# Kernel optimization log

Hardware: AMD Instinct MI355X
Metric: run time of the kernel (lower is better)

The kernel has to match this reference:

```python
import jax, jax.numpy as jnp
import numpy as np

B, T = 256, 64
ACT, EMB = 6, 1024
S, D = 32, 32          # stoch, discrete
SF = S * D             # flattened stochastic state (1024)
DET, HID = 600, 600


def _st_sample(logit, g):
    """Gumbel-max categorical sample with straight-through gradient.
    logit, g: [B, S, D]. Returns one-hot sample [B, S, D]."""
    idx = jnp.argmax(logit + g, axis=-1)
    onehot = jax.nn.one_hot(idx, logit.shape[-1], dtype=logit.dtype)
    probs = jax.nn.softmax(logit, axis=-1)
    return onehot + probs - jax.lax.stop_gradient(probs)


def setup_inputs() -> dict:
    key = jax.random.key(0)
    ks = jax.random.split(key, 20)
    p = lambda k, shp: (jax.random.normal(k, shp, dtype=jnp.float32) * 0.02)
    inp = {
        "action": jax.random.normal(ks[0], (B, T, ACT), dtype=jnp.float32),
        "embed": jax.random.normal(ks[1], (B, T, EMB), dtype=jnp.float32),
        "noise_img": jax.random.gumbel(ks[2], (B, T, S, D), dtype=jnp.float32),
        "noise_obs": jax.random.gumbel(ks[3], (B, T, S, D), dtype=jnp.float32),
        # img1: Dense(hidden, elu) on concat([stoch, action])
        "W_img1": p(ks[4], (SF + ACT, HID)), "b_img1": jnp.zeros((HID,), jnp.float32),
        # keras GRUCell (reset_after=True): gate order z, r, h; two biases
        "Wx": p(ks[5], (HID, 3 * DET)), "Wh": p(ks[6], (DET, 3 * DET)),
        "b_in": jnp.zeros((3 * DET,), jnp.float32), "b_rec": jnp.zeros((3 * DET,), jnp.float32),
        # img2: Dense(hidden, elu); img5: Dense(stoch*discrete)
        "W_img2": p(ks[7], (DET, HID)), "b_img2": jnp.zeros((HID,), jnp.float32),
        "W_img5": p(ks[8], (HID, SF)), "b_img5": jnp.zeros((SF,), jnp.float32),
        # obs1: Dense(hidden, elu) on concat([deter, embed]); obs3: Dense(stoch*discrete)
        "W_obs1": p(ks[9], (DET + EMB, HID)), "b_obs1": jnp.zeros((HID,), jnp.float32),
        "W_obs3": p(ks[10], (HID, SF)), "b_obs3": jnp.zeros((SF,), jnp.float32),
    }
    return inp


def reference(action, embed, noise_img, noise_obs,
              W_img1, b_img1, Wx, Wh, b_in, b_rec,
              W_img2, b_img2, W_img5, b_img5,
              W_obs1, b_obs1, W_obs3, b_obs3):
    # initial state: zeros (RSSM.initial)
    stoch0 = jnp.zeros((B, SF), jnp.float32)
    deter0 = jnp.zeros((B, DET), jnp.float32)

    def step(carry, inp):
        stoch, deter = carry                       # [B,SF], [B,DET]
        a, e, g_img, g_obs = inp
        # ---- img_step (prior) ----
        x = jax.nn.elu(jnp.concatenate([stoch, a], -1) @ W_img1 + b_img1)  # [B,HID]
        gx = x @ Wx + b_in                         # [B,3*DET]
        gh = deter @ Wh + b_rec
        xz, xr, xh = jnp.split(gx, 3, -1)
        hz, hr, hh = jnp.split(gh, 3, -1)
        z = jax.nn.sigmoid(xz + hz)
        r = jax.nn.sigmoid(xr + hr)
        cand = jnp.tanh(xh + r * hh)
        deter_n = z * deter + (1.0 - z) * cand     # [B,DET]
        y = jax.nn.elu(deter_n @ W_img2 + b_img2)
        logit_prior = (y @ W_img5 + b_img5).reshape(B, S, D)
        stoch_prior = _st_sample(logit_prior, g_img).reshape(B, SF)
        # ---- obs_step (post) ----
        o = jax.nn.elu(jnp.concatenate([deter_n, e], -1) @ W_obs1 + b_obs1)
        logit_post = (o @ W_obs3 + b_obs3).reshape(B, S, D)
        stoch_post = _st_sample(logit_post, g_obs).reshape(B, SF)
        out = (logit_post.reshape(B, SF), stoch_post, deter_n,
               logit_prior.reshape(B, SF), stoch_prior)
        return (stoch_post, deter_n), out

    xs = (jnp.swapaxes(action, 0, 1), jnp.swapaxes(embed, 0, 1),
          jnp.swapaxes(noise_img, 0, 1), jnp.swapaxes(noise_obs, 0, 1))
    _, outs = jax.lax.scan(step, (stoch0, deter0), xs)
    # outs: each [T,B,*] -> [B,T,*]; concat post_logit|post_stoch|deter|prior_logit|prior_stoch
    out = jnp.concatenate([jnp.swapaxes(o, 0, 1) for o in outs], axis=-1)  # [B,T,4*SF+DET]
    return out
```

## Files before the change

### kernel.cpp

```cpp
#include <hip/hip_runtime.h>
#include <math.h>

namespace {

constexpr int B = 256, T = 64, ACTN = 6, EMB = 1024;
constexpr int S = 32, DD = 32, SFN = 1024;
constexpr int DET = 600, HID = 600;
constexpr int OUTF = 4 * SFN + DET;

__device__ __forceinline__ float elu1(float x) { return x > 0.f ? x : expm1f(x); }
__device__ __forceinline__ float sigm(float x) { return 1.f / (1.f + expf(-x)); }

__device__ __forceinline__ bool jgMap(int bid, int& jg, int& rg) {
    int xcd = bid & 7, slot = bid >> 3;
    int jgLocal = slot >> 2;
    rg = slot & 3;
    int cnt = (xcd < 3) ? 10 : 9;
    if (jgLocal >= cnt) return false;
    jg = ((xcd < 3) ? xcd * 10 : 30 + (xcd - 3) * 9) + jgLocal;
    return true;
}

__global__ void kWB(const float* __restrict__ Wx, const float* __restrict__ Wh,
                    float* __restrict__ WBm) {
    int k = blockIdx.x;
    const float* src = (k < 600) ? (Wx + (size_t)k * 1800) : (Wh + (size_t)(k - 600) * 1800);
    for (int j = threadIdx.x; j < 600; j += blockDim.x) {
        size_t o = ((size_t)j * 1200 + k) * 3;
        WBm[o + 0] = src[j];
        WBm[o + 1] = src[600 + j];
        WBm[o + 2] = src[1200 + j];
    }
}

__global__ void kWC(const float* __restrict__ W2, const float* __restrict__ Wo1,
                    float* __restrict__ WCm) {
    int k = blockIdx.x;
    for (int j = threadIdx.x; j < 1200; j += blockDim.x) {
        float v = (j < 600) ? W2[(size_t)k * 600 + j] : Wo1[(size_t)k * 600 + (j - 600)];
        WCm[(size_t)j * 600 + k] = v;
    }
}

__global__ void kWD(const float* __restrict__ W5, const float* __restrict__ Wo3,
                    float* __restrict__ WDm) {
    int k = blockIdx.x;
    for (int j = threadIdx.x; j < 2048; j += blockDim.x) {
        float v = (j < 1024) ? W5[(size_t)k * 1024 + j] : Wo3[(size_t)k * 1024 + (j - 1024)];
        WDm[(size_t)j * 600 + k] = v;
    }
}

__global__ __launch_bounds__(512) void kPemb(const float* __restrict__ embed,
                                             const float* __restrict__ Wo1,
                                             const float* __restrict__ bo1,
                                             float* __restrict__ embPre) {
    int bid = blockIdx.x;
    int jg = bid % 10;
    int r = bid / 10;
    int bg = r & 3;
    int t = r >> 2;
    int tid = threadIdx.x;
    int lane = tid & 63;
    int wid = __builtin_amdgcn_readfirstlane(tid >> 6);
    int b0 = bg * 64;
    int j0 = jg * 64 + wid * 8;
    bool active = (j0 < 600);
    __shared__ float tile[64 * 129];
    float acc[8] = {0, 0, 0, 0, 0, 0, 0, 0};
    for (int kc = 0; kc < EMB; kc += 128) {
        __syncthreads();
        for (int ii = tid; ii < 64 * 128; ii += 512) {
            int i = ii >> 7, k = ii & 127;
            tile[i * 129 + k] = embed[((size_t)(b0 + i) * T + t) * EMB + kc + k];
        }
        __syncthreads();
        if (active) {
            const float* wbase = Wo1 + (size_t)(600 + kc) * 600 + j0;
#pragma unroll 4
            for (int k = 0; k < 128; ++k) {
                float v = tile[lane * 129 + k];
                float4 wa = *(const float4*)(wbase + (size_t)k * 600);
                float4 wb = *(const float4*)(wbase + (size_t)k * 600 + 4);
                acc[0] += v * wa.x; acc[1] += v * wa.y; acc[2] += v * wa.z; acc[3] += v * wa.w;
                acc[4] += v * wb.x; acc[5] += v * wb.y; acc[6] += v * wb.z; acc[7] += v * wb.w;
            }
        }
    }
    if (active) {
#pragma unroll
        for (int c = 0; c < 8; ++c)
            embPre[((size_t)t * 600 + j0 + c) * B + b0 + lane] = acc[c] + bo1[j0 + c];
    }
}

__global__ __launch_bounds__(256) void kA(const float* __restrict__ act,
                                          const float* __restrict__ W1,
                                          const float* __restrict__ b1,
                                          const int* __restrict__ idxB,
                                          float* __restrict__ xT, int t, int first) {
    int b = blockIdx.x, tid = threadIdx.x;
    __shared__ float sa[ACTN];
    __shared__ int si[S];
    if (tid < ACTN) sa[tid] = act[((size_t)b * T + t) * ACTN + tid];
    if (!first && tid < S) si[tid] = idxB[b * S + tid];
    __syncthreads();
    for (int h = tid; h < HID; h += 256) {
        float a = b1[h];
#pragma unroll
        for (int k = 0; k < ACTN; ++k) a += sa[k] * W1[(size_t)(SFN + k) * HID + h];
        if (!first) {
#pragma unroll 8
            for (int s = 0; s < S; ++s) a += W1[(size_t)(s * DD + si[s]) * HID + h];
        }
        xT[(size_t)h * B + b] = elu1(a);
    }
}

__global__ __launch_bounds__(512) void kB(const float* __restrict__ xT,
                                          const float* __restrict__ dPrev,
                                          const float* __restrict__ WBm,
                                          const float* __restrict__ b_in,
                                          const float* __restrict__ b_rec,
                                          float* __restrict__ dNext,
                                          float* __restrict__ out, int t) {
    int tid = threadIdx.x, lane = tid & 63;
    int wid = __builtin_amdgcn_readfirstlane(tid >> 6);
    int jg, rg;
    if (!jgMap(blockIdx.x, jg, rg)) return;
    int j = jg * 8 + wid;
    int b = rg * 64 + lane;
    const float* w = WBm + (size_t)j * 3600;
    float az = 0, ar = 0, ax = 0, ah = 0;
#pragma unroll 2
    for (int k = 0; k < 600; k += 4) {
        float4 wa = *(const float4*)(w + 3 * k);
        float4 wb = *(const float4*)(w + 3 * k + 4);
        float4 wc = *(const float4*)(w + 3 * k + 8);
        float x0 = xT[(size_t)(k + 0) * B + b];
        float x1 = xT[(size_t)(k + 1) * B + b];
        float x2 = xT[(size_t)(k + 2) * B + b];
        float x3 = xT[(size_t)(k + 3) * B + b];
        az += x0 * wa.x + x1 * wa.w + x2 * wb.z + x3 * wc.y;
        ar += x0 * wa.y + x1 * wb.x + x2 * wb.w + x3 * wc.z;
        ax += x0 * wa.z + x1 * wb.y + x2 * wc.x + x3 * wc.w;
    }
    const float* w2 = w + 1800;
#pragma unroll 2
    for (int k = 0; k < 600; k += 4) {
        float4 wa = *(const float4*)(w2 + 3 * k);
        float4 wb = *(const float4*)(w2 + 3 * k + 4);
        float4 wc = *(const float4*)(w2 + 3 * k + 8);
        float x0 = dPrev[(size_t)(k + 0) * B + b];
        float x1 = dPrev[(size_t)(k + 1) * B + b];
        float x2 = dPrev[(size_t)(k + 2) * B + b];
        float x3 = dPrev[(size_t)(k + 3) * B + b];
        az += x0 * wa.x + x1 * wa.w + x2 * wb.z + x3 * wc.y;
        ar += x0 * wa.y + x1 * wb.x + x2 * wb.w + x3 * wc.z;
        ah += x0 * wa.z + x1 * wb.y + x2 * wc.x + x3 * wc.w;
    }
    float dp = dPrev[(size_t)j * B + b];
    float z = sigm(az + b_in[j] + b_rec[j]);
    float rr = sigm(ar + b_in[600 + j] + b_rec[600 + j]);
    float cand = tanhf(ax + b_in[1200 + j] + rr * (ah + b_rec[1200 + j]));
    float dn = z * dp + (1.f - z) * cand;
    dNext[(size_t)j * B + b] = dn;
    out[((size_t)b * T + t) * OUTF + 2 * SFN + j] = dn;
}

__global__ __launch_bounds__(512) void kC(const float* __restrict__ dT,
                                          const float* __restrict__ WCm,
                                          const float* __restrict__ b2,
                                          const float* __restrict__ embPre,
                                          float* __restrict__ yoT, int t) {
    int tid = threadIdx.x, lane = tid & 63;
    int wid = __builtin_amdgcn_readfirstlane(tid >> 6);
    int jg, rg;
    if (!jgMap(blockIdx.x, jg, rg)) return;
    int j0 = jg * 16 + wid * 2;
    int b = rg * 64 + lane;
    const float* w0 = WCm + (size_t)j0 * 600;
    const float* w1 = w0 + 600;
    float a0 = 0, a1 = 0;
#pragma unroll 2
    for (int k = 0; k < 600; k += 4) {
        float4 p = *(const float4*)(w0 + k);
        float4 q = *(const float4*)(w1 + k);
        float v0 = dT[(size_t)(k + 0) * B + b];
        float v1 = dT[(size_t)(k + 1) * B + b];
        float v2 = dT[(size_t)(k + 2) * B + b];
        float v3 = dT[(size_t)(k + 3) * B + b];
        a0 += v0 * p.x + v1 * p.y + v2 * p.z + v3 * p.w;
        a1 += v0 * q.x + v1 * q.y + v2 * q.z + v3 * q.w;
    }
    if (j0 < 600) {
        yoT[(size_t)j0 * B + b] = elu1(a0 + b2[j0]);
        yoT[(size_t)(j0 + 1) * B + b] = elu1(a1 + b2[j0 + 1]);
    } else {
        int je = j0 - 600;
        yoT[(size_t)j0 * B + b] = elu1(a0 + embPre[((size_t)t * 600 + je) * B + b]);
        yoT[(size_t)(j0 + 1) * B + b] = elu1(a1 + embPre[((size_t)t * 600 + je + 1) * B + b]);
    }
}

__global__ __launch_bounds__(512) void kD(const float* __restrict__ yoT,
                                          const float* __restrict__ WDm,
                                          const float* __restrict__ b5,
                                          const float* __restrict__ bo3,
                                          const float* __restrict__ gImg,
                                          const float* __restrict__ gObs,
                                          float* __restrict__ out,
                                          int* __restrict__ idxB, int t) {
    int tid = threadIdx.x, lane = tid & 63;
    int wid = __builtin_amdgcn_readfirstlane(tid >> 6);
    int xcd = blockIdx.x & 7, slot = blockIdx.x >> 3;
    int sg = xcd * 8 + (slot & 7);
    int rg = slot >> 3;
    int post = (sg >= 32) ? 1 : 0;
    int s = post ? sg - 32 : sg;
    int b = rg * 64 + lane;
    int dloc = wid * 4;
    int jglob = post * SFN + s * DD + dloc;
    const float* src = yoT + (post ? (size_t)600 * B : 0);
    const float* w0 = WDm + (size_t)jglob * 600;
    const float* w1 = w0 + 600;
    const float* w2 = w0 + 1200;
    const float* w3 = w0 + 1800;
    float a0 = 0, a1 = 0, a2 = 0, a3 = 0;
#pragma unroll 2
    for (int k = 0; k < 600; k += 4) {
        float4 p0 = *(const float4*)(w0 + k);
        float4 p1 = *(const float4*)(w1 + k);
        float4 p2 = *(const float4*)(w2 + k);
        float4 p3 = *(const float4*)(w3 + k);
        float v0 = src[(size_t)(k + 0) * B + b];
        float v1 = src[(size_t)(k + 1) * B + b];
        float v2 = src[(size_t)(k + 2) * B + b];
        float v3 = src[(size_t)(k + 3) * B + b];
        a0 += v0 * p0.x + v1 * p0.y + v2 * p0.z + v3 * p0.w;
        a1 += v0 * p1.x + v1 * p1.y + v2 * p1.z + v3 * p1.w;
        a2 += v0 * p2.x + v1 * p2.y + v2 * p2.z + v3 * p2.w;
        a3 += v0 * p3.x + v1 * p3.y + v2 * p3.z + v3 * p3.w;
    }
    const float* bias = post ? (bo3 + s * DD) : (b5 + s * DD);
    const float* g = (post ? gObs : gImg) + ((size_t)b * T + t) * SFN + s * DD;
    size_t obase = ((size_t)b * T + t) * OUTF;
    size_t lbase = obase + (post ? 0 : (2 * SFN + DET)) + s * DD;
    float vals[4];
    float accs[4] = {a0, a1, a2, a3};
#pragma unroll
    for (int c = 0; c < 4; ++c) {
        float lg = accs[c] + bias[dloc + c];
        out[lbase + dloc + c] = lg;
        vals[c] = lg + g[dloc + c];
    }
    float bm = vals[0];
    int bi = dloc;
#pragma unroll
    for (int c = 1; c < 4; ++c)
        if (vals[c] > bm) { bm = vals[c]; bi = dloc + c; }
    __shared__ float sm[8 * 64];
    __shared__ int sx[8 * 64];
    sm[wid * 64 + lane] = bm;
    sx[wid * 64 + lane] = bi;
    __syncthreads();
    float best = sm[lane];
    int bd = sx[lane];
#pragma unroll
    for (int w = 1; w < 8; ++w) {
        float v = sm[w * 64 + lane];
        if (v > best) { best = v; bd = sx[w * 64 + lane]; }
    }
    size_t sbase = obase + (post ? SFN : (3 * SFN + DET)) + s * DD;
#pragma unroll
    for (int c = 0; c < 4; ++c)
        out[sbase + dloc + c] = (dloc + c == bd) ? 1.f : 0.f;
    if (post && wid == 0) idxB[b * S + s] = bd;
}

}

extern "C" void kernel_launch(void* const* d_in, const int* in_sizes, int n_in,
                              void* d_out, int out_size, void* d_ws, size_t ws_size,
                              hipStream_t stream) {
    const float* action = (const float*)d_in[0];
    const float* embed  = (const float*)d_in[1];
    const float* gImg   = (const float*)d_in[2];
    const float* gObs   = (const float*)d_in[3];
    const float* W1     = (const float*)d_in[4];
    const float* b1     = (const float*)d_in[5];
    const float* Wx     = (const float*)d_in[6];
    const float* Wh     = (const float*)d_in[7];
    const float* b_in   = (const float*)d_in[8];
    const float* b_rec  = (const float*)d_in[9];
    const float* W2     = (const float*)d_in[10];
    const float* b2     = (const float*)d_in[11];
    const float* W5     = (const float*)d_in[12];
    const float* b5     = (const float*)d_in[13];
    const float* Wo1    = (const float*)d_in[14];
    const float* bo1    = (const float*)d_in[15];
    const float* Wo3    = (const float*)d_in[16];
    const float* bo3    = (const float*)d_in[17];
    float* out = (float*)d_out;

    float* ws = (float*)d_ws;
    float* WBm    = ws;
    float* WCm    = WBm + 2160000;
    float* WDm    = WCm + 720000;
    float* embPre = WDm + 1228800;
    float* xT     = embPre + 9830400;
    float* dA     = xT + 153600;
    float* dB     = dA + 153600;
    float* yoT    = dB + 153600;
    int*   idxB   = (int*)(yoT + 307200);

    hipMemsetAsync(dA, 0, 153600 * sizeof(float), stream);
    kWB<<<1200, 256, 0, stream>>>(Wx, Wh, WBm);
    kWC<<<600, 256, 0, stream>>>(W2, Wo1, WCm);
    kWD<<<600, 256, 0, stream>>>(W5, Wo3, WDm);
    kPemb<<<2560, 512, 0, stream>>>(embed, Wo1, bo1, embPre);

    for (int t = 0; t < T; ++t) {
        float* dP = (t & 1) ? dB : dA;
        float* dN = (t & 1) ? dA : dB;
        kA<<<256, 256, 0, stream>>>(action, W1, b1, idxB, xT, t, t == 0 ? 1 : 0);
        kB<<<320, 512, 0, stream>>>(xT, dP, WBm, b_in, b_rec, dN, out, t);
        kC<<<320, 512, 0, stream>>>(dN, WCm, b2, embPre, yoT, t);
        kD<<<256, 512, 0, stream>>>(yoT, WDm, b5, bo3, gImg, gObs, out, idxB, t);
    }
}
```

Before: 10.32 ms.

## Split K across two wave halves and stage activations through LDS in GEMV kernels

The three per-step matvec kernels kB, kC and kD now launch 1024-thread blocks. Each K-range is split between two groups of 8 waves, and the partial sums are reduced through shared memory. Activation columns for the block's 64 batch rows are staged into LDS in chunks of 100 rows instead of being loaded per lane from global memory. The intent is more parallelism per output and fewer redundant global activation loads, at the cost of extra barriers, an LDS reduction, and tighter register limits from launch_bounds(1024,8).

```diff
diff --git a/kernel.cpp b/kernel.cpp
--- a/kernel.cpp
+++ b/kernel.cpp
@@ -7,6 +7,7 @@
 constexpr int S = 32, DD = 32, SFN = 1024;
 constexpr int DET = 600, HID = 600;
 constexpr int OUTF = 4 * SFN + DET;
+constexpr int KC = 100;
 
 __device__ __forceinline__ float elu1(float x) { return x > 0.f ? x : expm1f(x); }
 __device__ __forceinline__ float sigm(float x) { return 1.f / (1.f + expf(-x)); }
@@ -19,6 +20,21 @@
     if (jgLocal >= cnt) return false;
     jg = ((xcd < 3) ? xcd * 10 : 30 + (xcd - 3) * 9) + jgLocal;
     return true;
+}
+
+__device__ __forceinline__ void stage2(const float* __restrict__ sA,
+                                       const float* __restrict__ sB,
+                                       float* __restrict__ tA,
+                                       float* __restrict__ tB,
+                                       int b0, int tid) {
+    for (int idx = tid; idx < KC * 16 * 2; idx += 1024) {
+        int hf = idx >= KC * 16;
+        int i2 = hf ? (idx - KC * 16) : idx;
+        int kk = i2 >> 4, q = (i2 & 15) << 2;
+        float4 v = *(const float4*)((hf ? sB : sA) + (size_t)kk * B + b0 + q);
+        float* d = (hf ? tB : tA) + kk * 64 + q;
+        d[0] = v.x; d[1] = v.y; d[2] = v.z; d[3] = v.w;
+    }
 }
 
 __global__ void kWB(const float* __restrict__ Wx, const float* __restrict__ Wh,
@@ -117,165 +133,220 @@
     }
 }
 
-__global__ __launch_bounds__(512) void kB(const float* __restrict__ xT,
-                                          const float* __restrict__ dPrev,
-                                          const float* __restrict__ WBm,
-                                          const float* __restrict__ b_in,
-                                          const float* __restrict__ b_rec,
-                                          float* __restrict__ dNext,
-                                          float* __restrict__ out, int t) {
+__global__ __launch_bounds__(1024, 8) void kB(const float* __restrict__ xT,
+                                              const float* __restrict__ dPrev,
+                                              const float* __restrict__ WBm,
+                                              const float* __restrict__ b_in,
+                                              const float* __restrict__ b_rec,
+                                              float* __restrict__ dNext,
+                                              float* __restrict__ out, int t) {
+    int jg, rg;
+    if (!jgMap(blockIdx.x, jg, rg)) return;
     int tid = threadIdx.x, lane = tid & 63;
     int wid = __builtin_amdgcn_readfirstlane(tid >> 6);
+    int ws = wid & 7, kh = wid >> 3;
+    int j = jg * 8 + ws;
+    int b0 = rg * 64;
+    int b = b0 + lane;
+    __shared__ float tA[KC * 64];
+    __shared__ float tB[KC * 64];
+    __shared__ float part[8][3][64];
+    const float* wbase = WBm + (size_t)j * 3600 + (kh ? 1800 : 0);
+    float a0 = 0, a1 = 0, a2 = 0;
+    for (int c = 0; c < 600; c += KC) {
+        stage2(xT + (size_t)c * B, dPrev + (size_t)c * B, tA, tB, b0, tid);
+        __syncthreads();
+        const float* w = wbase + 3 * c;
+        const float* tl = kh ? tB : tA;
+#pragma unroll 2
+        for (int kk = 0; kk < KC; kk += 4) {
+            float4 wa = *(const float4*)(w + 3 * kk);
+            float4 wb = *(const float4*)(w + 3 * kk + 4);
+            float4 wc = *(const float4*)(w + 3 * kk + 8);
+            float x0 = tl[(kk + 0) * 64 + lane];
+            float x1 = tl[(kk + 1) * 64 + lane];
+            float x2 = tl[(kk + 2) * 64 + lane];
+            float x3 = tl[(kk + 3) * 64 + lane];
+            a0 += x0 * wa.x + x1 * wa.w + x2 * wb.z + x3 * wc.y;
+            a1 += x0 * wa.y + x1 * wb.x + x2 * wb.w + x3 * wc.z;
+            a2 += x0 * wa.z + x1 * wb.y + x2 * wc.x + x3 * wc.w;
+        }
+        __syncthreads();
+    }
+    if (kh) {
+        part[ws][0][lane] = a0;
+        part[ws][1][lane] = a1;
+        part[ws][2][lane] = a2;
+    }
+    __syncthreads();
+    if (!kh) {
+        float az = a0 + part[ws][0][lane];
+        float ar = a1 + part[ws][1][lane];
+        float ax = a2;
+        float ah = part[ws][2][lane];
+        float dp = dPrev[(size_t)j * B + b];
+        float z = sigm(az + b_in[j] + b_rec[j]);
+        float rr = sigm(ar + b_in[600 + j] + b_rec[600 + j]);
+        float cand = tanhf(ax + b_in[1200 + j] + rr * (ah + b_rec[1200 + j]));
+        float dn = z * dp + (1.f - z) * cand;
+        dNext[(size_t)j * B + b] = dn;
+        out[((size_t)b * T + t) * OUTF + 2 * SFN + j] = dn;
+    }
+}
+
+__global__ __launch_bounds__(1024, 8) void kC(const float* __restrict__ dT,
+                                              const float* __restrict__ WCm,
+                                              const float* __restrict__ b2,
+                                              const float* __restrict__ embPre,
+                                              float* __restrict__ yoT, int t) {
     int jg, rg;
     if (!jgMap(blockIdx.x, jg, rg)) return;
-    int j = jg * 8 + wid;
-    int b = rg * 64 + lane;
-    const float* w = WBm + (size_t)j * 3600;
-    float az = 0, ar = 0, ax = 0, ah = 0;
-#pragma unroll 2
-    for (int k = 0; k < 600; k += 4) {
-        float4 wa = *(const float4*)(w + 3 * k);
-        float4 wb = *(const float4*)(w + 3 * k + 4);
-        float4 wc = *(const float4*)(w + 3 * k + 8);
-        float x0 = xT[(size_t)(k + 0) * B + b];
-        float x1 = xT[(size_t)(k + 1) * B + b];
-        float x2 = xT[(size_t)(k + 2) * B + b];
-        float x3 = xT[(size_t)(k + 3) * B + b];
-        az += x0 * wa.x + x1 * wa.w + x2 * wb.z + x3 * wc.y;
-        ar += x0 * wa.y + x1 * wb.x + x2 * wb.w + x3 * wc.z;
-        ax += x0 * wa.z + x1 * wb.y + x2 * wc.x + x3 * wc.w;
-    }
-    const float* w2 = w + 1800;
-#pragma unroll 2
-    for (int k = 0; k < 600; k += 4) {
-        float4 wa = *(const float4*)(w2 + 3 * k);
-        float4 wb = *(const float4*)(w2 + 3 * k + 4);
-        float4 wc = *(const float4*)(w2 + 3 * k + 8);
-        float x0 = dPrev[(size_t)(k + 0) * B + b];
-        float x1 = dPrev[(size_t)(k + 1) * B + b];
-        float x2 = dPrev[(size_t)(k + 2) * B + b];
-        float x3 = dPrev[(size_t)(k + 3) * B + b];
-        az += x0 * wa.x + x1 * wa.w + x2 * wb.z + x3 * wc.y;
-        ar += x0 * wa.y + x1 * wb.x + x2 * wb.w + x3 * wc.z;
-        ah += x0 * wa.z + x1 * wb.y + x2 * wc.x + x3 * wc.w;
-    }
-    float dp = dPrev[(size_t)j * B + b];
-    float z = sigm(az + b_in[j] + b_rec[j]);
-    float rr = sigm(ar + b_in[600 + j] + b_rec[600 + j]);
-    float cand = tanhf(ax + b_in[1200 + j] + rr * (ah + b_rec[1200 + j]));
-    float dn = z * dp + (1.f - z) * cand;
-    dNext[(size_t)j * B + b] = dn;
-    out[((size_t)b * T + t) * OUTF + 2 * SFN + j] = dn;
-}
-
-__global__ __launch_bounds__(512) void kC(const float* __restrict__ dT,
-                                          const float* __restrict__ WCm,
-                                          const float* __restrict__ b2,
-                                          const float* __restrict__ embPre,
-                                          float* __restrict__ yoT, int t) {
     int tid = threadIdx.x, lane = tid & 63;
     int wid = __builtin_amdgcn_readfirstlane(tid >> 6);
-    int jg, rg;
-    if (!jgMap(blockIdx.x, jg, rg)) return;
-    int j0 = jg * 16 + wid * 2;
-    int b = rg * 64 + lane;
-    const float* w0 = WCm + (size_t)j0 * 600;
+    int ws = wid & 7, kh = wid >> 3;
+    int j0 = jg * 16 + ws * 2;
+    int b0 = rg * 64;
+    int b = b0 + lane;
+    __shared__ float tA[KC * 64];
+    __shared__ float tB[KC * 64];
+    __shared__ float part[8][2][64];
+    const float* w0 = WCm + (size_t)j0 * 600 + kh * 300;
     const float* w1 = w0 + 600;
     float a0 = 0, a1 = 0;
+    for (int c = 0; c < 300; c += KC) {
+        stage2(dT + (size_t)c * B, dT + (size_t)(300 + c) * B, tA, tB, b0, tid);
+        __syncthreads();
+        const float* tl = kh ? tB : tA;
 #pragma unroll 2
-    for (int k = 0; k < 600; k += 4) {
-        float4 p = *(const float4*)(w0 + k);
-        float4 q = *(const float4*)(w1 + k);
-        float v0 = dT[(size_t)(k + 0) * B + b];
-        float v1 = dT[(size_t)(k + 1) * B + b];
-        float v2 = dT[(size_t)(k + 2) * B + b];
-        float v3 = dT[(size_t)(k + 3) * B + b];
-        a0 += v0 * p.x + v1 * p.y + v2 * p.z + v3 * p.w;
-        a1 += v0 * q.x + v1 * q.y + v2 * q.z + v3 * q.w;
-    }
-    if (j0 < 600) {
-        yoT[(size_t)j0 * B + b] = elu1(a0 + b2[j0]);
-        yoT[(size_t)(j0 + 1) * B + b] = elu1(a1 + b2[j0 + 1]);
-    } else {
-        int je = j0 - 600;
-        yoT[(size_t)j0 * B + b] = elu1(a0 + embPre[((size_t)t * 600 + je) * B + b]);
-        yoT[(size_t)(j0 + 1) * B + b] = elu1(a1 + embPre[((size_t)t * 600 + je + 1) * B + b]);
-    }
-}
-
-__global__ __launch_bounds__(512) void kD(const float* __restrict__ yoT,
-                                          const float* __restrict__ WDm,
-                                          const float* __restrict__ b5,
-                                          const float* __restrict__ bo3,
-                                          const float* __restrict__ gImg,
-                                          const float* __restrict__ gObs,
-                                          float* __restrict__ out,
-                                          int* __restrict__ idxB, int t) {
+        for (int kk = 0; kk < KC; kk += 4) {
+            float4 p = *(const float4*)(w0 + c + kk);
+            float4 q = *(const float4*)(w1 + c + kk);
+            float v0 = tl[(kk + 0) * 64 + lane];
+            float v1 = tl[(kk + 1) * 64 + lane];
+            float v2 = tl[(kk + 2) * 64 + lane];
+            float v3 = tl[(kk + 3) * 64 + lane];
+            a0 += v0 * p.x + v1 * p.y + v2 * p.z + v3 * p.w;
+            a1 += v0 * q.x + v1 * q.y + v2 * q.z + v3 * q.w;
+        }
+        __syncthreads();
+    }
+    if (kh) {
+        part[ws][0][lane] = a0;
+        part[ws][1][lane] = a1;
+    }
+    __syncthreads();
+    if (!kh) {
+        float s0 = a0 + part[ws][0][lane];
+        float s1 = a1 + part[ws][1][lane];
+        if (j0 < 600) {
+            yoT[(size_t)j0 * B + b] = elu1(s0 + b2[j0]);
+            yoT[(size_t)(j0 + 1) * B + b] = elu1(s1 + b2[j0 + 1]);
+        } else {
+            int je = j0 - 600;
+            yoT[(size_t)j0 * B + b] = elu1(s0 + embPre[((size_t)t * 600 + je) * B + b]);
+            yoT[(size_t)(j0 + 1) * B + b] = elu1(s1 + embPre[((size_t)t * 600 + je + 1) * B + b]);
+        }
+    }
+}
+
+__global__ __launch_bounds__(1024, 4) void kD(const float* __restrict__ yoT,
+                                              const float* __restrict__ WDm,
+                                              const float* __restrict__ b5,
+                                              const float* __restrict__ bo3,
+                                              const float* __restrict__ gImg,
+                                              const float* __restrict__ gObs,
+                                              float* __restrict__ out,
+                                              int* __restrict__ idxB, int t) {
     int tid = threadIdx.x, lane = tid & 63;
     int wid = __builtin_amdgcn_readfirstlane(tid >> 6);
+    int ws = wid & 7, kh = wid >> 3;
     int xcd = blockIdx.x & 7, slot = blockIdx.x >> 3;
     int sg = xcd * 8 + (slot & 7);
     int rg = slot >> 3;
     int post = (sg >= 32) ? 1 : 0;
     int s = post ? sg - 32 : sg;
-    int b = rg * 64 + lane;
-    int dloc = wid * 4;
+    int b0 = rg * 64;
+    int b = b0 + lane;
+    int dloc = ws * 4;
     int jglob = post * SFN + s * DD + dloc;
     const float* src = yoT + (post ? (size_t)600 * B : 0);
-    const float* w0 = WDm + (size_t)jglob * 600;
+    __shared__ float tA[KC * 64];
+    __shared__ float tB[KC * 64];
+    __shared__ float part[8][4][64];
+    __shared__ float sm[8 * 64];
+    __shared__ int sx[8 * 64];
+    const float* w0 = WDm + (size_t)jglob * 600 + kh * 300;
     const float* w1 = w0 + 600;
     const float* w2 = w0 + 1200;
     const float* w3 = w0 + 1800;
     float a0 = 0, a1 = 0, a2 = 0, a3 = 0;
+    for (int c = 0; c < 300; c += KC) {
+        stage2(src + (size_t)c * B, src + (size_t)(300 + c) * B, tA, tB, b0, tid);
+        __syncthreads();
+        const float* tl = kh ? tB : tA;
 #pragma unroll 2
-    for (int k = 0; k < 600; k += 4) {
-        float4 p0 = *(const float4*)(w0 + k);
-        float4 p1 = *(const float4*)(w1 + k);
-        float4 p2 = *(const float4*)(w2 + k);
-        float4 p3 = *(const float4*)(w3 + k);
-        float v0 = src[(size_t)(k + 0) * B + b];
-        float v1 = src[(size_t)(k + 1) * B + b];
-        float v2 = src[(size_t)(k + 2) * B + b];
-        float v3 = src[(size_t)(k + 3) * B + b];
-        a0 += v0 * p0.x + v1 * p0.y + v2 * p0.z + v3 * p0.w;
-        a1 += v0 * p1.x + v1 * p1.y + v2 * p1.z + v3 * p1.w;
-        a2 += v0 * p2.x + v1 * p2.y + v2 * p2.z + v3 * p2.w;
-        a3 += v0 * p3.x + v1 * p3.y + v2 * p3.z + v3 * p3.w;
-    }
-    const float* bias = post ? (bo3 + s * DD) : (b5 + s * DD);
-    const float* g = (post ? gObs : gImg) + ((size_t)b * T + t) * SFN + s * DD;
-    size_t obase = ((size_t)b * T + t) * OUTF;
-    size_t lbase = obase + (post ? 0 : (2 * SFN + DET)) + s * DD;
-    float vals[4];
-    float accs[4] = {a0, a1, a2, a3};
-#pragma unroll
-    for (int c = 0; c < 4; ++c) {
-        float lg = accs[c] + bias[dloc + c];
-        out[lbase + dloc + c] = lg;
-        vals[c] = lg + g[dloc + c];
-    }
-    float bm = vals[0];
-    int bi = dloc;
-#pragma unroll
-    for (int c = 1; c < 4; ++c)
-        if (vals[c] > bm) { bm = vals[c]; bi = dloc + c; }
-    __shared__ float sm[8 * 64];
-    __shared__ int sx[8 * 64];
-    sm[wid * 64 + lane] = bm;
-    sx[wid * 64 + lane] = bi;
+        for (int kk = 0; kk < KC; kk += 4) {
+            float4 p0 = *(const float4*)(w0 + c + kk);
+            float4 p1 = *(const float4*)(w1 + c + kk);
+            float4 p2 = *(const float4*)(w2 + c + kk);
+            float4 p3 = *(const float4*)(w3 + c + kk);
+            float v0 = tl[(kk + 0) * 64 + lane];
+            float v1 = tl[(kk + 1) * 64 + lane];
+            float v2 = tl[(kk + 2) * 64 + lane];
+            float v3 = tl[(kk + 3) * 64 + lane];
+            a0 += v0 * p0.x + v1 * p0.y + v2 * p0.z + v3 * p0.w;
+            a1 += v0 * p1.x + v1 * p1.y + v2 * p1.z + v3 * p1.w;
+            a2 += v0 * p2.x + v1 * p2.y + v2 * p2.z + v3 * p2.w;
+            a3 += v0 * p3.x + v1 * p3.y + v2 * p3.z + v3 * p3.w;
+        }
+        __syncthreads();
+    }
+    if (kh) {
+        part[ws][0][lane] = a0;
+        part[ws][1][lane] = a1;
+        part[ws][2][lane] = a2;
+        part[ws][3][lane] = a3;
+    }
     __syncthreads();
-    float best = sm[lane];
-    int bd = sx[lane];
-#pragma unroll
-    for (int w = 1; w < 8; ++w) {
-        float v = sm[w * 64 + lane];
-        if (v > best) { best = v; bd = sx[w * 64 + lane]; }
-    }
-    size_t sbase = obase + (post ? SFN : (3 * SFN + DET)) + s * DD;
-#pragma unroll
-    for (int c = 0; c < 4; ++c)
-        out[sbase + dloc + c] = (dloc + c == bd) ? 1.f : 0.f;
-    if (post && wid == 0) idxB[b * S + s] = bd;
+    if (!kh) {
+        float accs[4] = {a0 + part[ws][0][lane], a1 + part[ws][1][lane],
+                         a2 + part[ws][2][lane], a3 + part[ws][3][lane]};
+        const float* bias = post ? (bo3 + s * DD) : (b5 + s * DD);
+        const float* g = (post ? gObs : gImg) + ((size_t)b * T + t) * SFN + s * DD;
+        size_t obase = ((size_t)b * T + t) * OUTF;
+        size_t lbase = obase + (post ? 0 : (2 * SFN + DET)) + s * DD;
+        float vals[4];
+#pragma unroll
+        for (int c = 0; c < 4; ++c) {
+            float lg = accs[c] + bias[dloc + c];
+            out[lbase + dloc + c] = lg;
+            vals[c] = lg + g[dloc + c];
+        }
+        float bm = vals[0];
+        int bi = dloc;
+#pragma unroll
+        for (int c = 1; c < 4; ++c)
+            if (vals[c] > bm) { bm = vals[c]; bi = dloc + c; }
+        sm[ws * 64 + lane] = bm;
+        sx[ws * 64 + lane] = bi;
+    }
+    __syncthreads();
+    if (!kh) {
+        float best = sm[lane];
+        int bd = sx[lane];
+#pragma unroll
+        for (int w = 1; w < 8; ++w) {
+            float v = sm[w * 64 + lane];
+            if (v > best) { best = v; bd = sx[w * 64 + lane]; }
+        }
+        int post2 = post;
+        size_t obase = ((size_t)b * T + t) * OUTF;
+        size_t sbase = obase + (post2 ? SFN : (3 * SFN + DET)) + s * DD;
+#pragma unroll
+        for (int c = 0; c < 4; ++c)
+            out[sbase + dloc + c] = (dloc + c == bd) ? 1.f : 0.f;
+        if (post2 && ws == 0) idxB[b * S + s] = bd;
+    }
 }
 
 }
@@ -324,8 +395,8 @@
         float* dP = (t & 1) ? dB : dA;
         float* dN = (t & 1) ? dA : dB;
         kA<<<256, 256, 0, stream>>>(action, W1, b1, idxB, xT, t, t == 0 ? 1 : 0);
-        kB<<<320, 512, 0, stream>>>(xT, dP, WBm, b_in, b_rec, dN, out, t);
-        kC<<<320, 512, 0, stream>>>(dN, WCm, b2, embPre, yoT, t);
-        kD<<<256, 512, 0, stream>>>(yoT, WDm, b5, bo3, gImg, gObs, out, idxB, t);
-    }
-}
+        kB<<<320, 1024, 0, stream>>>(xT, dP, WBm, b_in, b_rec, dN, out, t);
+        kC<<<320, 1024, 0, stream>>>(dN, WCm, b2, embPre, yoT, t);
+        kD<<<256, 1024, 0, stream>>>(yoT, WDm, b5, bo3, gImg, gObs, out, idxB, t);
+    }
+}
```

Result: faster. 9.135 ms (-11.5%).
